# Kernel optimization log

Measured on AMD Instinct MI355X. Metric: run time of the kernel, lower is better.

Reference implementation:

```python
import jax, jax.numpy as jnp
import numpy as np

# ---- module hyperparameters (from init_kwargs) ----
DIM = 16        # Hilbert-space dimension (density matrix is DIM x DIM)
BATCH = 32      # number of initial states evolved in parallel
K_LIND = 4      # number of Lindblad collapse operators
N_TS = 512      # number of Euler integration steps
N_CTRLS = 4     # number of control channels
N_PARAMS = 16   # B-spline control points per channel
DEGREE = 3      # cubic B-splines
T_TOTAL = 1.0
DT = T_TOTAL / N_TS


def _bspline_basis_matrix(t, knots, degree):
    """Cox-de Boor recursion, vectorized over all basis functions.
    t: (n_ts,), knots: (n_knots,). Returns (n_ts, n_knots-1-degree)."""
    k = knots
    # degree-0: indicator of half-open knot spans -> (n_ts, n_knots-1)
    B = ((k[None, :-1] <= t[:, None]) & (t[:, None] < k[None, 1:])).astype(t.dtype)
    for d in range(1, degree + 1):
        left_den = k[d:-1] - k[:-(d + 1)]
        right_den = k[d + 1:] - k[1:-d]
        left = jnp.where(left_den > 0,
                         (t[:, None] - k[None, :-(d + 1)]) / jnp.where(left_den > 0, left_den, 1.0) * B[:, :-1],
                         0.0)
        right = jnp.where(right_den > 0,
                          (k[None, d + 1:] - t[:, None]) / jnp.where(right_den > 0, right_den, 1.0) * B[:, 1:],
                          0.0)
        B = left + right
    return B  # (n_ts, n_knots - 1 - degree) == (n_ts, N_PARAMS)


def setup_inputs() -> dict:
    key = jax.random.key(0)
    ks = jax.random.split(key, 10)
    f32 = jnp.float32
    params = 0.5 * jax.random.normal(ks[0], (N_PARAMS, N_CTRLS), f32)
    H0_re = jax.random.normal(ks[1], (DIM, DIM), f32)
    H0_im = jax.random.normal(ks[2], (DIM, DIM), f32)
    Hc_re = jax.random.normal(ks[3], (N_CTRLS, DIM, DIM), f32)
    Hc_im = jax.random.normal(ks[4], (N_CTRLS, DIM, DIM), f32)
    L_re = 0.3 * jax.random.normal(ks[5], (K_LIND, DIM, DIM), f32)
    L_im = 0.3 * jax.random.normal(ks[6], (K_LIND, DIM, DIM), f32)
    # valid density matrices: rho0 = A A^dag / tr(A A^dag)
    A = (jax.random.normal(ks[7], (BATCH, DIM, DIM), f32)
         + 1j * jax.random.normal(ks[8], (BATCH, DIM, DIM), f32)).astype(jnp.complex64)
    rho0 = jnp.einsum('bij,bkj->bik', A, A.conj())
    tr = jnp.trace(rho0, axis1=-2, axis2=-1).real[:, None, None]
    rho0 = rho0 / tr.astype(jnp.complex64)
    return {
        'params': params,
        'H0_re': H0_re, 'H0_im': H0_im,
        'Hc_re': Hc_re, 'Hc_im': Hc_im,
        'L_re': L_re, 'L_im': L_im,
        'rho0_re': jnp.real(rho0).astype(f32),
        'rho0_im': jnp.imag(rho0).astype(f32),
    }


def reference(params, H0_re, H0_im, Hc_re, Hc_im, L_re, L_im, rho0_re, rho0_im):
    c64 = jnp.complex64
    # Hermitize Hamiltonians
    H0 = (H0_re + 1j * H0_im).astype(c64)
    H0 = 0.5 * (H0 + H0.conj().T)
    Hc = (Hc_re + 1j * Hc_im).astype(c64)
    Hc = 0.5 * (Hc + jnp.conj(jnp.swapaxes(Hc, -1, -2)))
    L = (L_re + 1j * L_im).astype(c64)              # (K, d, d)
    LdL = jnp.einsum('kji,kjl->il', L.conj(), L)    # sum_k L^dag L  (d, d)
    rho0 = (rho0_re + 1j * rho0_im).astype(c64)     # (B, d, d)

    # B-spline control pulses (clamped knot vector, as in evaluate_bspline_batch)
    t = jnp.arange(N_TS, dtype=jnp.float32) * DT
    knots = jnp.concatenate([
        jnp.zeros(DEGREE, jnp.float32),
        jnp.linspace(0.0, T_TOTAL, N_PARAMS - DEGREE + 1).astype(jnp.float32),
        T_TOTAL * jnp.ones(DEGREE, jnp.float32),
    ])
    basis = _bspline_basis_matrix(t, knots, DEGREE)  # (n_ts, n_params)
    u = basis @ params                               # (n_ts, n_ctrls)

    def step(rho, u_t):
        H = H0 + jnp.einsum('c,cij->ij', u_t.astype(c64), Hc)
        jump = jnp.einsum('kij,bjl,kml->bim', L, rho, L.conj())
        drho = (-1j) * (H @ rho - rho @ H) + jump - 0.5 * (LdL @ rho + rho @ LdL)
        rho_new = rho + DT * drho
        pops = jnp.real(jnp.diagonal(rho_new, axis1=-2, axis2=-1)).astype(jnp.float32)
        return rho_new, pops

    _, pops = jax.lax.scan(step, rho0, u)
    return pops  # (n_ts, batch, dim) real populations
```

## Files before the change

### kernel.cpp

```cpp
#include <hip/hip_runtime.h>
#include <hip/hip_bf16.h>

#define DIM    16
#define BATCH  32
#define KL     4
#define NTS    512
#define NC     4
#define NPAR   16
#define DTF    (1.0f/512.0f)
#define BST    40

using short8  = __attribute__((ext_vector_type(8))) short;
using short4v = __attribute__((ext_vector_type(4))) short;
using f32x4   = __attribute__((ext_vector_type(4))) float;

__device__ __forceinline__ float b2f(__hip_bfloat16 x) { return __bfloat162float(x); }

__device__ __forceinline__ float ldval(const void* p, int idx, bool isf32) {
  return isf32 ? ((const float*)p)[idx]
               : __bfloat162float(((const __hip_bfloat16*)p)[idx]);
}
__device__ __forceinline__ unsigned short f2bf(float x) {
  unsigned u = __float_as_uint(x);
  unsigned r = u + 0x7FFFu + ((u >> 16) & 1u);
  return (unsigned short)(r >> 16);
}
__device__ __forceinline__ float bf2f(unsigned short h) {
  return __uint_as_float(((unsigned)h) << 16);
}
__device__ __forceinline__ void split2(float v, unsigned short& h, unsigned short& l) {
  unsigned u = __float_as_uint(v);
  h = (unsigned short)(u >> 16);
  float r = v - __uint_as_float(u & 0xFFFF0000u);
  l = (unsigned short)(__float_as_uint(r) >> 16);
}
__device__ __forceinline__ short8 ldfrag(const unsigned short* p) {
  return *(const short8*)p;
}
__device__ __forceinline__ short8 negbf8(short8 a) {
  union { short8 s; unsigned u[4]; } v; v.s = a;
  #pragma unroll
  for (int q = 0; q < 4; ++q) v.u[q] ^= 0x80008000u;
  return v.s;
}
__device__ __forceinline__ f32x4 mm3(short8 Ah, short8 Al, short8 Bh, short8 Bl, f32x4 acc) {
  acc = __builtin_amdgcn_mfma_f32_16x16x32_bf16(Ah, Bh, acc, 0, 0, 0);
  acc = __builtin_amdgcn_mfma_f32_16x16x32_bf16(Al, Bh, acc, 0, 0, 0);
  acc = __builtin_amdgcn_mfma_f32_16x16x32_bf16(Ah, Bl, acc, 0, 0, 0);
  return acc;
}
__device__ __forceinline__ f32x4 mm3b(short8 Ah, short8 Al, short8 Bh, short8 Bl, f32x4 acc) {
  acc = __builtin_amdgcn_mfma_f32_16x16x32_bf16(Ah, Bh, acc, 0, 0, 0);
  acc = __builtin_amdgcn_mfma_f32_16x16x32_bf16(Ah, Bl, acc, 0, 0, 0);
  acc = __builtin_amdgcn_mfma_f32_16x16x32_bf16(Al, Bh, acc, 0, 0, 0);
  return acc;
}
__device__ __forceinline__ void pack4(f32x4 v, short4v& hi, short4v& lo) {
  union { short4v s; unsigned d[2]; } H, L;
  unsigned u0 = __float_as_uint(v[0]), u1 = __float_as_uint(v[1]);
  unsigned u2 = __float_as_uint(v[2]), u3 = __float_as_uint(v[3]);
  H.d[0] = __builtin_amdgcn_perm(u1, u0, 0x07060302u);
  H.d[1] = __builtin_amdgcn_perm(u3, u2, 0x07060302u);
  float r0 = v[0] - __uint_as_float(u0 & 0xFFFF0000u);
  float r1 = v[1] - __uint_as_float(u1 & 0xFFFF0000u);
  float r2 = v[2] - __uint_as_float(u2 & 0xFFFF0000u);
  float r3 = v[3] - __uint_as_float(u3 & 0xFFFF0000u);
  L.d[0] = __builtin_amdgcn_perm(__float_as_uint(r1), __float_as_uint(r0), 0x07060302u);
  L.d[1] = __builtin_amdgcn_perm(__float_as_uint(r3), __float_as_uint(r2), 0x07060302u);
  hi = H.s; lo = L.s;
}
__device__ __forceinline__ void pack8(const float* v, short8& hi, short8& lo) {
  union { short8 s; unsigned d[4]; } H, L;
  #pragma unroll
  for (int j = 0; j < 4; ++j) {
    unsigned ua = __float_as_uint(v[2*j]), ub = __float_as_uint(v[2*j+1]);
    H.d[j] = __builtin_amdgcn_perm(ub, ua, 0x07060302u);
    float ra = v[2*j]   - __uint_as_float(ua & 0xFFFF0000u);
    float rb = v[2*j+1] - __uint_as_float(ub & 0xFFFF0000u);
    L.d[j] = __builtin_amdgcn_perm(__float_as_uint(rb), __float_as_uint(ra), 0x07060302u);
  }
  hi = H.s; lo = L.s;
}

__global__ __launch_bounds__(384, 1)
void lindblad_evolve(const void* __restrict__ g_params,
                     const void* __restrict__ g_H0re, const void* __restrict__ g_H0im,
                     const void* __restrict__ g_Hcre, const void* __restrict__ g_Hcim,
                     const void* __restrict__ g_Lre,  const void* __restrict__ g_Lim,
                     const void* __restrict__ g_r0re, const void* __restrict__ g_r0im,
                     float* __restrict__ g_out)
{
  __shared__ __align__(16) unsigned short sPh[16*BST], sPl[16*BST];
  __shared__ __align__(16) unsigned short sTh[KL][16*BST], sTl[KL][16*BST];
  __shared__ __align__(16) unsigned short sLh[KL][16*BST], sLl[KL][16*BST];
  __shared__ __align__(16) float sU[NTS][NC];
  __shared__ __align__(16) float sPops[NTS*DIM];
  __shared__ int sFlag;

  const int tid = threadIdx.x;
  const int b   = blockIdx.x;
  const int wv  = tid >> 6;
  const int ln  = tid & 63;
  const int fm  = ln & 15;
  const int fq  = ln >> 4;
  const int row0 = fq * 4;
  const int fOff  = fm*BST + fq*8;
  const int fOffS = fm*BST + ((fq*8 + 16) & 31);

  if (tid == 0) sFlag = 0;
  __syncthreads();
  if (tid < 256) {
    float v = b2f(((const __hip_bfloat16*)g_H0re)[tid]);
    if (!(fabsf(v) <= 1e10f)) atomicOr(&sFlag, 1);
  }
  __syncthreads();
  const bool isf32 = (sFlag != 0);

  for (int t0 = tid; t0 < NTS; t0 += 384) {
    float kn[20];
    kn[0] = 0.f; kn[1] = 0.f; kn[2] = 0.f;
    #pragma unroll
    for (int q = 0; q < 14; ++q) kn[3 + q] = (float)q / 13.0f;
    kn[17] = 1.f; kn[18] = 1.f; kn[19] = 1.f;
    const float t = (float)t0 * DTF;
    float B[19];
    #pragma unroll
    for (int q = 0; q < 19; ++q) B[q] = (kn[q] <= t && t < kn[q+1]) ? 1.f : 0.f;
    #pragma unroll
    for (int d = 1; d <= 3; ++d) {
      #pragma unroll
      for (int q = 0; q + d < 19; ++q) {
        float ld = kn[q+d]   - kn[q];
        float rd = kn[q+d+1] - kn[q+1];
        float lv = (ld > 0.f) ? (t - kn[q])     / ld * B[q]   : 0.f;
        float rv = (rd > 0.f) ? (kn[q+d+1] - t) / rd * B[q+1] : 0.f;
        B[q] = lv + rv;
      }
    }
    #pragma unroll
    for (int c = 0; c < NC; ++c) {
      float s = 0.f;
      #pragma unroll
      for (int q = 0; q < NPAR; ++q) s += B[q] * ldval(g_params, q*NC + c, isf32);
      sU[t0][c] = s;
    }
  }

  if (tid < 256) {
    float* scr = sPops;
    const int i = tid >> 4, j = tid & 15;
    const int ij = i*16 + j, ji = j*16 + i;
    float h0r = 0.5f * (ldval(g_H0re, ij, isf32) + ldval(g_H0re, ji, isf32));
    float h0i = 0.5f * (ldval(g_H0im, ij, isf32) - ldval(g_H0im, ji, isf32));
    float ldr = 0.f, ldi = 0.f;
    for (int k = 0; k < KL; ++k) {
      #pragma unroll
      for (int m = 0; m < DIM; ++m) {
        float ar = ldval(g_Lre, k*256 + m*16 + i, isf32), ai = ldval(g_Lim, k*256 + m*16 + i, isf32);
        float br = ldval(g_Lre, k*256 + m*16 + j, isf32), bi = ldval(g_Lim, k*256 + m*16 + j, isf32);
        ldr += ar*br + ai*bi;
        ldi += ar*bi - ai*br;
      }
    }
    scr[0*256 + ij] =  h0i - 0.5f*ldr;
    scr[1*256 + ij] = -h0r - 0.5f*ldi;
    #pragma unroll
    for (int c = 0; c < NC; ++c) {
      float hr = 0.5f * (ldval(g_Hcre, c*256 + ij, isf32) + ldval(g_Hcre, c*256 + ji, isf32));
      float hi = 0.5f * (ldval(g_Hcim, c*256 + ij, isf32) - ldval(g_Hcim, c*256 + ji, isf32));
      scr[(2 + 2*c)*256 + ij] =  hi;
      scr[(3 + 2*c)*256 + ij] = -hr;
    }
    #pragma unroll
    for (int k = 0; k < KL; ++k) {
      float lr = ldval(g_Lre, k*256 + ij, isf32);
      float li = ldval(g_Lim, k*256 + ij, isf32);
      unsigned short h;
      h = f2bf(lr); sLh[k][i*BST + j]      = h; sLl[k][i*BST + j]      = f2bf(lr - bf2f(h));
      h = f2bf(li); sLh[k][i*BST + 16 + j] = h; sLl[k][i*BST + 16 + j] = f2bf(li - bf2f(h));
    }
    float r0 = ldval(g_r0re, b*256 + ij, isf32);
    float m0 = ldval(g_r0im, b*256 + ij, isf32);
    unsigned short h, l;
    split2(r0, h, l); sPh[j*BST + i]      = h; sPl[j*BST + i]      = l;
    split2(m0, h, l); sPh[j*BST + 16 + i] = h; sPl[j*BST + 16 + i] = l;
  }

  __syncthreads();

  short8 Ah, Al;
  short8 TrBh, TrBl, TiBh, TiBl;
  short8 JBh[KL], JBl[KL];
  float  G0v[8], Gcv[NC][8];
  float  rm[4] = {0.f,0.f,0.f,0.f};

  if (wv >= 4) {
    const int comp = (fq < 2) ? 0 : 1;
    const int base = (fq & 1) * 8;
    const float* scr = sPops;
    {
      const float* s0 = &scr[comp*256 + fm*16 + base];
      f32x4 va = *(const f32x4*)s0, vb = *(const f32x4*)(s0 + 4);
      #pragma unroll
      for (int q = 0; q < 4; ++q) { G0v[q] = va[q]; G0v[4+q] = vb[q]; }
    }
    #pragma unroll
    for (int c = 0; c < NC; ++c) {
      const float* s0 = &scr[(2 + 2*c + comp)*256 + fm*16 + base];
      f32x4 va = *(const f32x4*)s0, vb = *(const f32x4*)(s0 + 4);
      #pragma unroll
      for (int q = 0; q < 4; ++q) { Gcv[c][q] = va[q]; Gcv[c][4+q] = vb[q]; }
    }
    f32x4 uv = *(const f32x4*)&sU[0][0];
    float gv[8];
    #pragma unroll
    for (int q = 0; q < 8; ++q)
      gv[q] = G0v[q] + uv[0]*Gcv[0][q] + uv[1]*Gcv[1][q] + uv[2]*Gcv[2][q] + uv[3]*Gcv[3][q];
    pack8(gv, Ah, Al);
    if (wv == 4) {
      #pragma unroll
      for (int k = 0; k < KL; ++k) { JBh[k] = ldfrag(&sLh[k][fOff]); JBl[k] = ldfrag(&sLl[k][fOff]); }
      #pragma unroll
      for (int q = 0; q < 4; ++q) rm[q] = ldval(g_r0re, b*256 + (row0+q)*16 + fm, isf32);
    } else {
      #pragma unroll
      for (int k = 0; k < KL; ++k) {
        short8 h = ldfrag(&sLh[k][fOffS]);
        short8 l = ldfrag(&sLl[k][fOffS]);
        if (fq < 2) { h = negbf8(h); l = negbf8(l); }
        JBh[k] = h; JBl[k] = l;
      }
      #pragma unroll
      for (int q = 0; q < 4; ++q) rm[q] = ldval(g_r0im, b*256 + (row0+q)*16 + fm, isf32);
    }
  } else {
    const int k = wv;
    TiBh = ldfrag(&sLh[k][fOff]);
    TiBl = ldfrag(&sLl[k][fOff]);
    TrBh = (fq >= 2) ? negbf8(TiBh) : TiBh;
    TrBl = (fq >= 2) ? negbf8(TiBl) : TiBl;
  }

  const f32x4 zero = {0.f, 0.f, 0.f, 0.f};

  #pragma unroll 1
  for (int t = 0; t < NTS; ++t) {
    f32x4 mAcc, mtAcc;

    __syncthreads();

    if (wv < 4) {
      const int k = wv;
      short8 Arh = ldfrag(&sPh[fOff]),  Arl = ldfrag(&sPl[fOff]);
      short8 Aih = ldfrag(&sPh[fOffS]), Ail = ldfrag(&sPl[fOffS]);
      f32x4 tr = zero, ti = zero;
      tr = mm3(Arh, Arl, TrBh, TrBl, tr);
      ti = mm3(Aih, Ail, TiBh, TiBl, ti);
      short4v HR, LR, HI2, LI2;
      pack4(tr, HR, LR);
      pack4(ti, HI2, LI2);
      *(short4v*)&sTh[k][fm*BST + row0]      = HR;
      *(short4v*)&sTl[k][fm*BST + row0]      = LR;
      *(short4v*)&sTh[k][fm*BST + 16 + row0] = HI2;
      *(short4v*)&sTl[k][fm*BST + 16 + row0] = LI2;
    } else if (wv == 4) {
      short8 Ph = ldfrag(&sPh[fOff]), Pl = ldfrag(&sPl[fOff]);
      short8 Bh = (fq >= 2) ? negbf8(Ph) : Ph;
      short8 Bl = (fq >= 2) ? negbf8(Pl) : Pl;
      mAcc = mm3(Ah, Al, Bh, Bl, zero);
      short8 Gth = (fq >= 2) ? negbf8(Ah) : Ah;
      short8 Gtl = (fq >= 2) ? negbf8(Al) : Al;
      mtAcc = mm3b(Ph, Pl, Gth, Gtl, zero);
    } else {
      short8 Ph = ldfrag(&sPh[fOffS]), Pl = ldfrag(&sPl[fOffS]);
      mAcc = mm3(Ah, Al, Ph, Pl, zero);
      mtAcc = mm3b(Ph, Pl, Ah, Al, zero);
    }

    __syncthreads();

    if (wv >= 4) {
      short8 T0h = ldfrag(&sTh[0][fOff]), T0l = ldfrag(&sTl[0][fOff]);
      short8 T1h = ldfrag(&sTh[1][fOff]), T1l = ldfrag(&sTl[1][fOff]);
      short8 T2h = ldfrag(&sTh[2][fOff]), T2l = ldfrag(&sTl[2][fOff]);
      short8 T3h = ldfrag(&sTh[3][fOff]), T3l = ldfrag(&sTl[3][fOff]);
      f32x4 a0 = zero, a1 = zero, a2 = zero, a3 = zero;
      a0 = mm3(JBh[0], JBl[0], T0h, T0l, a0);
      a1 = mm3(JBh[1], JBl[1], T1h, T1l, a1);
      a2 = mm3(JBh[2], JBl[2], T2h, T2l, a2);
      a3 = mm3(JBh[3], JBl[3], T3h, T3l, a3);

      short4v HH, LL;
      f32x4 rv;
      if (wv == 4) {
        #pragma unroll
        for (int q = 0; q < 4; ++q) {
          rm[q] += DTF * (mAcc[q] + mtAcc[q] + ((a0[q] + a1[q]) + (a2[q] + a3[q])));
          rv[q] = rm[q];
        }
        pack4(rv, HH, LL);
        *(short4v*)&sPh[fm*BST + row0] = HH;
        *(short4v*)&sPl[fm*BST + row0] = LL;
        if ((unsigned)(fm - row0) < 4u) sPops[t*DIM + fm] = rm[fm - row0];
      } else {
        #pragma unroll
        for (int q = 0; q < 4; ++q) {
          rm[q] += DTF * (mAcc[q] - mtAcc[q] - ((a0[q] + a1[q]) + (a2[q] + a3[q])));
          rv[q] = rm[q];
        }
        pack4(rv, HH, LL);
        *(short4v*)&sPh[fm*BST + 16 + row0] = HH;
        *(short4v*)&sPl[fm*BST + 16 + row0] = LL;
      }

      const int tn = (t + 1 < NTS) ? (t + 1) : t;
      f32x4 uv = *(const f32x4*)&sU[tn][0];
      float gv[8];
      #pragma unroll
      for (int q = 0; q < 8; ++q)
        gv[q] = G0v[q] + uv[0]*Gcv[0][q] + uv[1]*Gcv[1][q] + uv[2]*Gcv[2][q] + uv[3]*Gcv[3][q];
      pack8(gv, Ah, Al);
    }
  }

  __syncthreads();
  for (int i4 = tid; i4 < NTS*DIM/4; i4 += 384) {
    int idx = i4 * 4;
    int tt = idx >> 4, dd = idx & 15;
    *(float4*)&g_out[tt*(BATCH*DIM) + b*DIM + dd] = *(const float4*)&sPops[idx];
  }
}

extern "C" void kernel_launch(void* const* d_in, const int* in_sizes, int n_in,
                              void* d_out, int out_size, void* d_ws, size_t ws_size,
                              hipStream_t stream) {
  (void)out_size; (void)d_ws; (void)ws_size;
  const void *P, *H0r, *H0i, *Hcr, *Hci, *Lr, *Li, *R0r, *R0i;
  int idx64 = -1;
  for (int q = 0; q < n_in; ++q) if (in_sizes[q] == 64) idx64 = q;
  if (idx64 == 6) {
    H0i = d_in[0]; H0r = d_in[1];
    Hci = d_in[2]; Hcr = d_in[3];
    Li  = d_in[4]; Lr  = d_in[5];
    P   = d_in[6];
    R0i = d_in[7]; R0r = d_in[8];
  } else {
    P   = d_in[0];
    H0r = d_in[1]; H0i = d_in[2];
    Hcr = d_in[3]; Hci = d_in[4];
    Lr  = d_in[5]; Li  = d_in[6];
    R0r = d_in[7]; R0i = d_in[8];
  }
  lindblad_evolve<<<dim3(BATCH), dim3(384), 0, stream>>>(
      P, H0r, H0i, Hcr, Hci, Lr, Li, R0r, R0i, (float*)d_out);
}
```

Before: 493.6 us.

## Move jump-term MFMAs into the four L-waves and share Hamiltonian via LDS

The four per-Lindblad-operator waves now also compute the second half of the jump product (L times the intermediate T) and write fp32 partial results to shared memory. The two update waves then only read and sum those partials instead of running four extra MFMA products on the serial critical path. Building the time-dependent Hamiltonian is moved to wave 0, which publishes it through shared memory during the update phase. This shortens the second phase of each step but lengthens the first, adds LDS traffic and relies on a write-then-read by the same wave with no barrier in between.

```diff
diff --git a/kernel.cpp b/kernel.cpp
--- a/kernel.cpp
+++ b/kernel.cpp
@@ -93,6 +93,8 @@
   __shared__ __align__(16) unsigned short sPh[16*BST], sPl[16*BST];
   __shared__ __align__(16) unsigned short sTh[KL][16*BST], sTl[KL][16*BST];
   __shared__ __align__(16) unsigned short sLh[KL][16*BST], sLl[KL][16*BST];
+  __shared__ __align__(16) unsigned short sGh[16*BST], sGl[16*BST];
+  __shared__ __align__(16) float sJr[KL][256], sJi[KL][256];
   __shared__ __align__(16) float sU[NTS][NC];
   __shared__ __align__(16) float sPops[NTS*DIM];
   __shared__ int sFlag;
@@ -188,57 +190,53 @@
 
   __syncthreads();
 
-  short8 Ah, Al;
-  short8 TrBh, TrBl, TiBh, TiBl;
-  short8 JBh[KL], JBl[KL];
+  short8 LFh_, LFl_, TrBh_, TrBl_, LSh_, LSl_;
   float  G0v[8], Gcv[NC][8];
   float  rm[4] = {0.f,0.f,0.f,0.f};
 
-  if (wv >= 4) {
-    const int comp = (fq < 2) ? 0 : 1;
-    const int base = (fq & 1) * 8;
-    const float* scr = sPops;
-    {
-      const float* s0 = &scr[comp*256 + fm*16 + base];
-      f32x4 va = *(const f32x4*)s0, vb = *(const f32x4*)(s0 + 4);
-      #pragma unroll
-      for (int q = 0; q < 4; ++q) { G0v[q] = va[q]; G0v[4+q] = vb[q]; }
-    }
-    #pragma unroll
-    for (int c = 0; c < NC; ++c) {
-      const float* s0 = &scr[(2 + 2*c + comp)*256 + fm*16 + base];
-      f32x4 va = *(const f32x4*)s0, vb = *(const f32x4*)(s0 + 4);
-      #pragma unroll
-      for (int q = 0; q < 4; ++q) { Gcv[c][q] = va[q]; Gcv[c][4+q] = vb[q]; }
-    }
-    f32x4 uv = *(const f32x4*)&sU[0][0];
-    float gv[8];
-    #pragma unroll
-    for (int q = 0; q < 8; ++q)
-      gv[q] = G0v[q] + uv[0]*Gcv[0][q] + uv[1]*Gcv[1][q] + uv[2]*Gcv[2][q] + uv[3]*Gcv[3][q];
-    pack8(gv, Ah, Al);
-    if (wv == 4) {
-      #pragma unroll
-      for (int k = 0; k < KL; ++k) { JBh[k] = ldfrag(&sLh[k][fOff]); JBl[k] = ldfrag(&sLl[k][fOff]); }
-      #pragma unroll
-      for (int q = 0; q < 4; ++q) rm[q] = ldval(g_r0re, b*256 + (row0+q)*16 + fm, isf32);
-    } else {
-      #pragma unroll
-      for (int k = 0; k < KL; ++k) {
-        short8 h = ldfrag(&sLh[k][fOffS]);
-        short8 l = ldfrag(&sLl[k][fOffS]);
-        if (fq < 2) { h = negbf8(h); l = negbf8(l); }
-        JBh[k] = h; JBl[k] = l;
-      }
-      #pragma unroll
-      for (int q = 0; q < 4; ++q) rm[q] = ldval(g_r0im, b*256 + (row0+q)*16 + fm, isf32);
-    }
+  if (wv < 4) {
+    const int k = wv;
+    LFh_ = ldfrag(&sLh[k][fOff]);
+    LFl_ = ldfrag(&sLl[k][fOff]);
+    TrBh_ = (fq >= 2) ? negbf8(LFh_) : LFh_;
+    TrBl_ = (fq >= 2) ? negbf8(LFl_) : LFl_;
+    short8 h = ldfrag(&sLh[k][fOffS]);
+    short8 l = ldfrag(&sLl[k][fOffS]);
+    if (fq < 2) { h = negbf8(h); l = negbf8(l); }
+    LSh_ = h; LSl_ = l;
+    if (wv == 0) {
+      const int comp = (fq < 2) ? 0 : 1;
+      const int base = (fq & 1) * 8;
+      const float* scr = sPops;
+      {
+        const float* s0 = &scr[comp*256 + fm*16 + base];
+        f32x4 va = *(const f32x4*)s0, vb = *(const f32x4*)(s0 + 4);
+        #pragma unroll
+        for (int q = 0; q < 4; ++q) { G0v[q] = va[q]; G0v[4+q] = vb[q]; }
+      }
+      #pragma unroll
+      for (int c = 0; c < NC; ++c) {
+        const float* s0 = &scr[(2 + 2*c + comp)*256 + fm*16 + base];
+        f32x4 va = *(const f32x4*)s0, vb = *(const f32x4*)(s0 + 4);
+        #pragma unroll
+        for (int q = 0; q < 4; ++q) { Gcv[c][q] = va[q]; Gcv[c][4+q] = vb[q]; }
+      }
+      f32x4 uv = *(const f32x4*)&sU[0][0];
+      float gv[8];
+      #pragma unroll
+      for (int q = 0; q < 8; ++q)
+        gv[q] = G0v[q] + uv[0]*Gcv[0][q] + uv[1]*Gcv[1][q] + uv[2]*Gcv[2][q] + uv[3]*Gcv[3][q];
+      short8 Gh_, Gl_;
+      pack8(gv, Gh_, Gl_);
+      *(short8*)&sGh[fm*BST + fq*8] = Gh_;
+      *(short8*)&sGl[fm*BST + fq*8] = Gl_;
+    }
+  } else if (wv == 4) {
+    #pragma unroll
+    for (int q = 0; q < 4; ++q) rm[q] = ldval(g_r0re, b*256 + (row0+q)*16 + fm, isf32);
   } else {
-    const int k = wv;
-    TiBh = ldfrag(&sLh[k][fOff]);
-    TiBl = ldfrag(&sLl[k][fOff]);
-    TrBh = (fq >= 2) ? negbf8(TiBh) : TiBh;
-    TrBl = (fq >= 2) ? negbf8(TiBl) : TiBl;
+    #pragma unroll
+    for (int q = 0; q < 4; ++q) rm[q] = ldval(g_r0im, b*256 + (row0+q)*16 + fm, isf32);
   }
 
   const f32x4 zero = {0.f, 0.f, 0.f, 0.f};
@@ -253,9 +251,8 @@
       const int k = wv;
       short8 Arh = ldfrag(&sPh[fOff]),  Arl = ldfrag(&sPl[fOff]);
       short8 Aih = ldfrag(&sPh[fOffS]), Ail = ldfrag(&sPl[fOffS]);
-      f32x4 tr = zero, ti = zero;
-      tr = mm3(Arh, Arl, TrBh, TrBl, tr);
-      ti = mm3(Aih, Ail, TiBh, TiBl, ti);
+      f32x4 tr = mm3(Arh, Arl, TrBh_, TrBl_, zero);
+      f32x4 ti = mm3(Aih, Ail, LFh_,  LFl_,  zero);
       short4v HR, LR, HI2, LI2;
       pack4(tr, HR, LR);
       pack4(ti, HI2, LI2);
@@ -263,7 +260,13 @@
       *(short4v*)&sTl[k][fm*BST + row0]      = LR;
       *(short4v*)&sTh[k][fm*BST + 16 + row0] = HI2;
       *(short4v*)&sTl[k][fm*BST + 16 + row0] = LI2;
+      short8 Th = ldfrag(&sTh[k][fOff]), Tl = ldfrag(&sTl[k][fOff]);
+      f32x4 jr = mm3(LFh_, LFl_, Th, Tl, zero);
+      f32x4 ji = mm3(LSh_, LSl_, Th, Tl, zero);
+      *(f32x4*)&sJr[k][ln*4] = jr;
+      *(f32x4*)&sJi[k][ln*4] = ji;
     } else if (wv == 4) {
+      short8 Ah = ldfrag(&sGh[fOff]), Al = ldfrag(&sGl[fOff]);
       short8 Ph = ldfrag(&sPh[fOff]), Pl = ldfrag(&sPl[fOff]);
       short8 Bh = (fq >= 2) ? negbf8(Ph) : Ph;
       short8 Bl = (fq >= 2) ? negbf8(Pl) : Pl;
@@ -272,6 +275,7 @@
       short8 Gtl = (fq >= 2) ? negbf8(Al) : Al;
       mtAcc = mm3b(Ph, Pl, Gth, Gtl, zero);
     } else {
+      short8 Ah = ldfrag(&sGh[fOff]), Al = ldfrag(&sGl[fOff]);
       short8 Ph = ldfrag(&sPh[fOffS]), Pl = ldfrag(&sPl[fOffS]);
       mAcc = mm3(Ah, Al, Ph, Pl, zero);
       mtAcc = mm3b(Ph, Pl, Ah, Al, zero);
@@ -280,16 +284,11 @@
     __syncthreads();
 
     if (wv >= 4) {
-      short8 T0h = ldfrag(&sTh[0][fOff]), T0l = ldfrag(&sTl[0][fOff]);
-      short8 T1h = ldfrag(&sTh[1][fOff]), T1l = ldfrag(&sTl[1][fOff]);
-      short8 T2h = ldfrag(&sTh[2][fOff]), T2l = ldfrag(&sTl[2][fOff]);
-      short8 T3h = ldfrag(&sTh[3][fOff]), T3l = ldfrag(&sTl[3][fOff]);
-      f32x4 a0 = zero, a1 = zero, a2 = zero, a3 = zero;
-      a0 = mm3(JBh[0], JBl[0], T0h, T0l, a0);
-      a1 = mm3(JBh[1], JBl[1], T1h, T1l, a1);
-      a2 = mm3(JBh[2], JBl[2], T2h, T2l, a2);
-      a3 = mm3(JBh[3], JBl[3], T3h, T3l, a3);
-
+      const float* sJ = (wv == 4) ? &sJr[0][0] : &sJi[0][0];
+      f32x4 a0 = *(const f32x4*)&sJ[0*256 + ln*4];
+      f32x4 a1 = *(const f32x4*)&sJ[1*256 + ln*4];
+      f32x4 a2 = *(const f32x4*)&sJ[2*256 + ln*4];
+      f32x4 a3 = *(const f32x4*)&sJ[3*256 + ln*4];
       short4v HH, LL;
       f32x4 rv;
       if (wv == 4) {
@@ -312,14 +311,17 @@
         *(short4v*)&sPh[fm*BST + 16 + row0] = HH;
         *(short4v*)&sPl[fm*BST + 16 + row0] = LL;
       }
-
+    } else if (wv == 0) {
       const int tn = (t + 1 < NTS) ? (t + 1) : t;
       f32x4 uv = *(const f32x4*)&sU[tn][0];
       float gv[8];
       #pragma unroll
       for (int q = 0; q < 8; ++q)
         gv[q] = G0v[q] + uv[0]*Gcv[0][q] + uv[1]*Gcv[1][q] + uv[2]*Gcv[2][q] + uv[3]*Gcv[3][q];
-      pack8(gv, Ah, Al);
+      short8 Gh_, Gl_;
+      pack8(gv, Gh_, Gl_);
+      *(short8*)&sGh[fm*BST + fq*8] = Gh_;
+      *(short8*)&sGl[fm*BST + fq*8] = Gl_;
     }
   }
 
```

New measurement: 417.8 us. -15.4%, faster.
